# Kernel tuning notes

Hardware: AMD Instinct MI355X
Metric: run time of the kernel (lower is better)

## Reference

```python
import jax, jax.numpy as jnp
import numpy as np

B, T, D, H = 4, 4096, 2048, 16
HD = D // H
CAPACITY = 0.125
K = max(1, int(T * CAPACITY))  # 512
D_FF = int(D * 4 * 2 / 3)      # 5461
EPS = 1e-6


def setup_inputs() -> dict:
    key = jax.random.key(0)
    ks = jax.random.split(key, 9)
    s = 0.02
    return {
        "x": jax.random.normal(ks[0], (B, T, D), jnp.float32),
        "position_ids": jnp.tile(jnp.arange(T, dtype=jnp.int32)[None, :], (B, 1)),
        "router_w": jax.random.normal(ks[1], (D,), jnp.float32) * s,
        "norm1_w": jnp.ones((D,), jnp.float32),
        "qkv_w": jax.random.normal(ks[2], (D, 3 * D), jnp.float32) * s,
        "out_w": jax.random.normal(ks[3], (D, D), jnp.float32) * s,
        "norm2_w": jnp.ones((D,), jnp.float32),
        "w1": jax.random.normal(ks[4], (D, D_FF), jnp.float32) * s,
        "w2": jax.random.normal(ks[5], (D, D_FF), jnp.float32) * s,
        "w3": jax.random.normal(ks[6], (D_FF, D), jnp.float32) * s,
    }


def _rmsnorm(x, w):
    return x * jax.lax.rsqrt(jnp.mean(x * x, axis=-1, keepdims=True) + EPS) * w


def _block(x, pos, norm1_w, qkv_w, out_w, norm2_w, w1, w2, w3):
    # x: (B, k, D), pos: (B, k) original positions
    b, t, d = x.shape
    h = _rmsnorm(x, norm1_w)
    qkv = (h @ qkv_w).reshape(b, t, 3, H, HD)
    q = jnp.moveaxis(qkv[:, :, 0], 2, 1)  # (b, H, t, HD)
    k = jnp.moveaxis(qkv[:, :, 1], 2, 1)
    v = jnp.moveaxis(qkv[:, :, 2], 2, 1)
    attn = jnp.einsum("bhqd,bhkd->bhqk", q, k) / jnp.sqrt(jnp.float32(HD))
    # causal mask on ORIGINAL positions: query pos_i attends only to pos_j <= pos_i
    mask = (pos[:, :, None] < pos[:, None, :])[:, None]  # (b,1,t,t) True = masked
    attn = jnp.where(mask, -jnp.inf, attn)
    attn = jax.nn.softmax(attn, axis=-1)
    attn = jnp.nan_to_num(attn, nan=0.0)
    o = jnp.einsum("bhqk,bhkd->bhqd", attn, v)
    o = jnp.moveaxis(o, 1, 2).reshape(b, t, d) @ out_w
    x = x + o
    h = _rmsnorm(x, norm2_w)
    ff = (jax.nn.silu(h @ w1) * (h @ w2)) @ w3
    return x + ff


def reference(x, position_ids, router_w, norm1_w, qkv_w, out_w, norm2_w, w1, w2, w3):
    b, t, d = x.shape
    scores = x @ router_w  # (B, T)
    tie = jnp.arange(t, dtype=x.dtype) * 1e-6
    _, top_idx = jax.lax.top_k(scores + tie[None, :], K)
    sorted_idx = jnp.sort(top_idx, axis=-1)  # (B, K)
    x_sel = jnp.take_along_axis(x, sorted_idx[:, :, None], axis=1)  # (B, K, D)
    pos_sel = jnp.take_along_axis(position_ids, sorted_idx, axis=1)  # (B, K)
    x_proc = _block(x_sel, pos_sel, norm1_w, qkv_w, out_w, norm2_w, w1, w2, w3)
    b_idx = jnp.arange(b)[:, None]
    output = x.at[b_idx, sorted_idx].set(x_proc)
    return output
```

## Files before the change

kernel.cpp:

```cpp
#include <hip/hip_runtime.h>
#include <hip/hip_bf16.h>

#define BB 4
#define TT 4096
#define DD 2048
#define HH 16
#define HDD 128
#define KSEL 512
#define DFF 5461
#define DFFP 5504

typedef __attribute__((ext_vector_type(8))) short short8;
typedef __attribute__((ext_vector_type(4))) float floatx4;

__device__ __forceinline__ void g2l16(const void* g, void* l) {
  __builtin_amdgcn_global_load_lds((const __attribute__((address_space(1))) void*)g,
                                   (__attribute__((address_space(3))) void*)l,
                                   16, 0, 0);
}

__global__ __launch_bounds__(256) void router_copy(
    const float* __restrict__ x, const float* __restrict__ rw,
    float* __restrict__ out, float* __restrict__ scores) {
  const long row = blockIdx.x;
  const long base = row * DD;
  const int tid = threadIdx.x;
  float s = 0.f;
#pragma unroll
  for (int it = 0; it < 2; ++it) {
    const int c = (tid + it * 256) * 4;
    const float4 v = *(const float4*)(x + base + c);
    *(float4*)(out + base + c) = v;
    const float4 w = *(const float4*)(rw + c);
    s += v.x * w.x + v.y * w.y + v.z * w.z + v.w * w.w;
  }
  __shared__ float red[256];
  red[tid] = s; __syncthreads();
  for (int st = 128; st > 0; st >>= 1) { if (tid < st) red[tid] += red[tid + st]; __syncthreads(); }
  if (tid == 0) scores[row] = red[0];
}

__global__ __launch_bounds__(256) void topk_select(
    const float* __restrict__ scores, int* __restrict__ idx_sel) {
  const int b = blockIdx.x;
  const int tid = threadIdx.x;
  __shared__ float key[TT];
  __shared__ float fred[256];
  __shared__ int ired[256];
  __shared__ int ia[256], ib[256];
  __shared__ float s_lo, s_hi;
  __shared__ int s_strict;
  const float* sc = scores + (long)b * TT;
  for (int t = tid; t < TT; t += 256) key[t] = sc[t] + (float)t * 1e-6f;
  __syncthreads();
  float mn = 1e30f, mx = -1e30f;
  for (int t = tid; t < TT; t += 256) { const float v = key[t]; mn = fminf(mn, v); mx = fmaxf(mx, v); }
  fred[tid] = mn; __syncthreads();
  for (int s = 128; s > 0; s >>= 1) { if (tid < s) fred[tid] = fminf(fred[tid], fred[tid + s]); __syncthreads(); }
  if (tid == 0) s_lo = fred[0] - 1.f;
  __syncthreads();
  fred[tid] = mx; __syncthreads();
  for (int s = 128; s > 0; s >>= 1) { if (tid < s) fred[tid] = fmaxf(fred[tid], fred[tid + s]); __syncthreads(); }
  if (tid == 0) s_hi = fred[0];
  __syncthreads();
  for (int it = 0; it < 64; ++it) {
    const float lo = s_lo, hi = s_hi;
    const float mid = 0.5f * (lo + hi);
    if (!(mid > lo && mid < hi)) break;
    int c = 0;
    for (int t = tid; t < TT; t += 256) c += (key[t] > mid) ? 1 : 0;
    ired[tid] = c; __syncthreads();
    for (int s = 128; s > 0; s >>= 1) { if (tid < s) ired[tid] += ired[tid + s]; __syncthreads(); }
    if (tid == 0) { if (ired[0] >= KSEL) s_lo = mid; else s_hi = mid; }
    __syncthreads();
  }
  const float hi = s_hi;
  const int t0c = tid * 16;
  int cs = 0, ce = 0;
  for (int t = t0c; t < t0c + 16; ++t) { const float v = key[t]; cs += (v > hi); ce += (v == hi); }
  ia[tid] = cs; ib[tid] = ce; __syncthreads();
  if (tid == 0) {
    int st = 0, et = 0;
    for (int i2 = 0; i2 < 256; ++i2) { const int a = ia[i2], e2 = ib[i2]; ia[i2] = st; ib[i2] = et; st += a; et += e2; }
    s_strict = st;
  }
  __syncthreads();
  const int neq = KSEL - s_strict;
  {
    int eqr = ib[tid];
    int sel = 0;
    for (int t = t0c; t < t0c + 16; ++t) {
      const float v = key[t];
      if (v > hi) sel++;
      else if (v == hi) { if (eqr < neq) sel++; eqr++; }
    }
    ired[tid] = sel;
  }
  __syncthreads();
  if (tid == 0) { int st = 0; for (int i2 = 0; i2 < 256; ++i2) { const int a = ired[i2]; ired[i2] = st; st += a; } }
  __syncthreads();
  {
    int pos = ired[tid];
    int eqr = ib[tid];
    for (int t = t0c; t < t0c + 16; ++t) {
      const float v = key[t];
      bool s = false;
      if (v > hi) s = true;
      else if (v == hi) { s = (eqr < neq); eqr++; }
      if (s) idx_sel[(long)b * KSEL + (pos++)] = t;
    }
  }
}

__global__ __launch_bounds__(256) void rmsnorm_rows(
    const float* __restrict__ src, const int* __restrict__ idx,
    const float* __restrict__ w, __hip_bfloat16* __restrict__ dst, int gather) {
  const int m = blockIdx.x;
  const int tid = threadIdx.x;
  const float* row;
  if (gather) {
    const int b = m >> 9;
    const int t = idx[m];
    row = src + ((long)b * TT + t) * DD;
  } else {
    row = src + (long)m * DD;
  }
  const float4 v0 = *(const float4*)(row + tid * 4);
  const float4 v1 = *(const float4*)(row + 1024 + tid * 4);
  float ss = v0.x * v0.x + v0.y * v0.y + v0.z * v0.z + v0.w * v0.w
           + v1.x * v1.x + v1.y * v1.y + v1.z * v1.z + v1.w * v1.w;
  __shared__ float red[256];
  __shared__ float s_r;
  red[tid] = ss; __syncthreads();
  for (int s = 128; s > 0; s >>= 1) { if (tid < s) red[tid] += red[tid + s]; __syncthreads(); }
  if (tid == 0) s_r = rsqrtf(red[0] * (1.f / (float)DD) + 1e-6f);
  __syncthreads();
  const float r = s_r;
  const float4 w0 = *(const float4*)(w + tid * 4);
  const float4 w1v = *(const float4*)(w + 1024 + tid * 4);
  __hip_bfloat16* drow = dst + (long)m * DD;
  const int c = tid * 4;
  drow[c + 0] = __float2bfloat16(v0.x * r * w0.x);
  drow[c + 1] = __float2bfloat16(v0.y * r * w0.y);
  drow[c + 2] = __float2bfloat16(v0.z * r * w0.z);
  drow[c + 3] = __float2bfloat16(v0.w * r * w0.w);
  drow[1024 + c + 0] = __float2bfloat16(v1.x * r * w1v.x);
  drow[1024 + c + 1] = __float2bfloat16(v1.y * r * w1v.y);
  drow[1024 + c + 2] = __float2bfloat16(v1.z * r * w1v.z);
  drow[1024 + c + 3] = __float2bfloat16(v1.w * r * w1v.w);
}

__global__ __launch_bounds__(256) void transpose_cast(
    const float* __restrict__ in, __hip_bfloat16* __restrict__ out,
    int R, int C, int Rp, int Cp) {
  __shared__ float tile[32][33];
  const int r0 = blockIdx.x * 32, c0 = blockIdx.y * 32;
  const int tx = threadIdx.x & 31, ty = threadIdx.x >> 5;
  for (int yy = ty; yy < 32; yy += 8) {
    const int r = r0 + yy, c = c0 + tx;
    tile[yy][tx] = (r < R && c < C) ? in[(long)r * C + c] : 0.f;
  }
  __syncthreads();
  for (int yy = ty; yy < 32; yy += 8) {
    const int c = c0 + yy, r = r0 + tx;
    if (c < Cp && r < Rp) out[(long)c * Rp + r] = __float2bfloat16(tile[tx][yy]);
  }
}

__global__ __launch_bounds__(256) void softmax_rows(
    const __hip_bfloat16* __restrict__ S, __hip_bfloat16* __restrict__ P) {
  const int row = blockIdx.x * 4 + (threadIdx.x >> 6);
  const int lane = threadIdx.x & 63;
  const int i = row & (KSEL - 1);
  const long base = (long)row * KSEL;
  float v[8];
  float mx = -1e30f;
#pragma unroll
  for (int e = 0; e < 8; ++e) {
    const int j = e * 64 + lane;
    const float s = (j <= i) ? __bfloat162float(S[base + j]) : -1e30f;
    v[e] = s; mx = fmaxf(mx, s);
  }
#pragma unroll
  for (int d = 32; d > 0; d >>= 1) mx = fmaxf(mx, __shfl_xor(mx, d, 64));
  float sum = 0.f;
#pragma unroll
  for (int e = 0; e < 8; ++e) { const float p = __expf(v[e] - mx); v[e] = p; sum += p; }
#pragma unroll
  for (int d = 32; d > 0; d >>= 1) sum += __shfl_xor(sum, d, 64);
  const float inv = 1.f / sum;
#pragma unroll
  for (int e = 0; e < 8; ++e) P[base + e * 64 + lane] = __float2bfloat16(v[e] * inv);
}

template <int EPI>
__global__ __launch_bounds__(256) void gemm_bt(
    const __hip_bfloat16* __restrict__ A,
    const __hip_bfloat16* __restrict__ B,
    const __hip_bfloat16* __restrict__ B2,
    int ntm, int ntn, int gmx, int gnx,
    int K, long bsA, long bsB, float scale,
    void* __restrict__ out0,
    const int* __restrict__ idx,
    const float* __restrict__ xres,
    __hip_bfloat16* __restrict__ qb,
    __hip_bfloat16* __restrict__ kb,
    __hip_bfloat16* __restrict__ vtb) {
  constexpr bool DUAL = (EPI == 3);
  __shared__ unsigned short As[128 * 32];
  __shared__ unsigned short Bs[128 * 32];
  __shared__ unsigned short Bs2[DUAL ? 128 * 32 : 8];

  const int z = blockIdx.z;
  int bm, bn;
  if (gmx > 0) {
    const int xcd = blockIdx.x & 7;
    const int j = blockIdx.x >> 3;
    const int xm = xcd % gmx, xn = xcd / gmx;
    const int m_lo = (xm * ntm) / gmx;
    const int m_cnt = ((xm + 1) * ntm) / gmx - m_lo;
    const int n_lo = (xn * ntn) / gnx;
    const int n_cnt = ((xn + 1) * ntn) / gnx - n_lo;
    if (j >= m_cnt * n_cnt) return;
    bm = m_lo + j % m_cnt;
    bn = n_lo + j / m_cnt;
  } else {
    bm = blockIdx.x / ntn;
    bn = blockIdx.x % ntn;
  }
  const int tid = threadIdx.x;

  const __hip_bfloat16* Ab = A + (long)z * bsA + (long)bm * 128 * K;
  const __hip_bfloat16* Bb = B + (long)z * bsB + (long)bn * 128 * K;

  const int m1 = tid >> 2;
  const int p8 = (tid & 3) * 8;

  const floatx4 zero4 = {0.f, 0.f, 0.f, 0.f};
  floatx4 acc[4][4];
  floatx4 acc2[4][4];
#pragma unroll
  for (int i = 0; i < 4; ++i)
#pragma unroll
    for (int j = 0; j < 4; ++j) { acc[i][j] = zero4; if constexpr (DUAL) acc2[i][j] = zero4; }

  const int lane = tid & 63;
  const int wave = tid >> 6;
  const int wm = (wave & 1) << 6;
  const int wn = (wave >> 1) << 6;
  const int lrow = lane & 15;
  const int kq = (lane >> 4) << 3;

  for (int k0 = 0; k0 < K; k0 += 32) {
    const __hip_bfloat16* ag = Ab + (long)m1 * K + (k0 + p8);
    g2l16(ag, &As[tid * 8]);
    g2l16(ag + (long)64 * K, &As[(tid + 256) * 8]);
    const __hip_bfloat16* bg = Bb + (long)m1 * K + (k0 + p8);
    g2l16(bg, &Bs[tid * 8]);
    g2l16(bg + (long)64 * K, &Bs[(tid + 256) * 8]);
    if constexpr (DUAL) {
      const __hip_bfloat16* b2g = B2 + (long)bn * 128 * K + (long)m1 * K + (k0 + p8);
      g2l16(b2g, &Bs2[tid * 8]);
      g2l16(b2g + (long)64 * K, &Bs2[(tid + 256) * 8]);
    }
    __syncthreads();
    short8 af[4], bfr[4];
#pragma unroll
    for (int i = 0; i < 4; ++i) af[i] = *(const short8*)&As[(wm + i * 16 + lrow) * 32 + kq];
#pragma unroll
    for (int j = 0; j < 4; ++j) bfr[j] = *(const short8*)&Bs[(wn + j * 16 + lrow) * 32 + kq];
#pragma unroll
    for (int i = 0; i < 4; ++i)
#pragma unroll
      for (int j = 0; j < 4; ++j)
        acc[i][j] = __builtin_amdgcn_mfma_f32_16x16x32_bf16(af[i], bfr[j], acc[i][j], 0, 0, 0);
    if constexpr (DUAL) {
      short8 bf2[4];
#pragma unroll
      for (int j = 0; j < 4; ++j) bf2[j] = *(const short8*)&Bs2[(wn + j * 16 + lrow) * 32 + kq];
#pragma unroll
      for (int i = 0; i < 4; ++i)
#pragma unroll
        for (int j = 0; j < 4; ++j)
          acc2[i][j] = __builtin_amdgcn_mfma_f32_16x16x32_bf16(af[i], bf2[j], acc2[i][j], 0, 0, 0);
    }
    __syncthreads();
  }

  const int cn = lane & 15;
  const int rb = (lane >> 4) << 2;
#pragma unroll
  for (int i = 0; i < 4; ++i) {
#pragma unroll
    for (int j = 0; j < 4; ++j) {
#pragma unroll
      for (int r = 0; r < 4; ++r) {
        const int gm = bm * 128 + wm + i * 16 + rb + r;
        const int gn = bn * 128 + wn + j * 16 + cn;
        const float v = acc[i][j][r];
        if constexpr (EPI == 0) {
          ((__hip_bfloat16*)out0)[(long)z * KSEL * KSEL + (long)gm * KSEL + gn] =
              __float2bfloat16(v * scale);
        } else if constexpr (EPI == 5) {
          const int b = z >> 4, h = z & 15;
          ((__hip_bfloat16*)out0)[((long)(b * KSEL + gm)) * DD + h * HDD + gn] =
              __float2bfloat16(v);
        } else if constexpr (EPI == 1) {
          const int b = gm >> 9, t = gm & 511;
          const int sec = gn >> 11, rem = gn & 2047, h = rem >> 7, hd = rem & 127;
          const __hip_bfloat16 val = __float2bfloat16(v);
          const long bh = (long)b * HH + h;
          if (sec == 0)      qb[(bh * KSEL + t) * HDD + hd] = val;
          else if (sec == 1) kb[(bh * KSEL + t) * HDD + hd] = val;
          else               vtb[(bh * HDD + hd) * KSEL + t] = val;
        } else if constexpr (EPI == 2) {
          const int b = gm >> 9;
          const int t0 = idx[gm];
          ((float*)out0)[(long)gm * DD + gn] = xres[((long)b * TT + t0) * DD + gn] + v;
        } else if constexpr (EPI == 3) {
          const float a1 = v;
          const float a2 = acc2[i][j][r];
          const float sgl = a1 / (1.f + __expf(-a1));
          ((__hip_bfloat16*)out0)[(long)gm * DFFP + gn] = __float2bfloat16(sgl * a2);
        } else if constexpr (EPI == 4) {
          const int b = gm >> 9;
          const int t0 = idx[gm];
          ((float*)out0)[((long)b * TT + t0) * DD + gn] = xres[(long)gm * DD + gn] + v;
        }
      }
    }
  }
}

extern "C" void kernel_launch(void* const* d_in, const int* in_sizes, int n_in,
                              void* d_out, int out_size, void* d_ws, size_t ws_size,
                              hipStream_t stream) {
  const float* x        = (const float*)d_in[0];
  const float* router_w = (const float*)d_in[2];
  const float* norm1_w  = (const float*)d_in[3];
  const float* qkv_w    = (const float*)d_in[4];
  const float* out_w    = (const float*)d_in[5];
  const float* norm2_w  = (const float*)d_in[6];
  const float* w1       = (const float*)d_in[7];
  const float* w2       = (const float*)d_in[8];
  const float* w3       = (const float*)d_in[9];
  float* out = (float*)d_out;

  char* wsb = (char*)d_ws;
  size_t off = 0;
  auto alloc = [&](size_t bytes) -> void* {
    void* p = wsb + off;
    off += (bytes + 255) & ~(size_t)255;
    return p;
  };
  float* scores = (float*)alloc((size_t)BB * TT * 4);
  int* idxs     = (int*)alloc((size_t)BB * KSEL * 4);
  __hip_bfloat16* qkvt = (__hip_bfloat16*)alloc((size_t)3 * DD * DD * 2);
  __hip_bfloat16* outt = (__hip_bfloat16*)alloc((size_t)DD * DD * 2);
  __hip_bfloat16* w1t  = (__hip_bfloat16*)alloc((size_t)DFFP * DD * 2);
  __hip_bfloat16* w2t  = (__hip_bfloat16*)alloc((size_t)DFFP * DD * 2);
  __hip_bfloat16* w3t  = (__hip_bfloat16*)alloc((size_t)DD * DFFP * 2);
  __hip_bfloat16* h1   = (__hip_bfloat16*)alloc((size_t)BB * KSEL * DD * 2);
  __hip_bfloat16* qbuf = (__hip_bfloat16*)alloc((size_t)BB * HH * KSEL * HDD * 2);
  __hip_bfloat16* kbuf = (__hip_bfloat16*)alloc((size_t)BB * HH * KSEL * HDD * 2);
  __hip_bfloat16* vtb  = (__hip_bfloat16*)alloc((size_t)BB * HH * KSEL * HDD * 2);
  __hip_bfloat16* Sbuf = (__hip_bfloat16*)alloc((size_t)BB * HH * KSEL * KSEL * 2);
  __hip_bfloat16* Pbuf = (__hip_bfloat16*)alloc((size_t)BB * HH * KSEL * KSEL * 2);
  __hip_bfloat16* obuf = h1;
  __hip_bfloat16* h2   = qbuf;
  __hip_bfloat16* ubuf = Pbuf;
  float* x1f           = (float*)Sbuf;
  (void)ws_size; (void)in_sizes; (void)n_in; (void)out_size;

  const float inv_sqrt_hd = 0.08838834764831845f;

  router_copy<<<dim3(BB * TT), dim3(256), 0, stream>>>(x, router_w, out, scores);
  topk_select<<<dim3(BB), dim3(256), 0, stream>>>(scores, idxs);
  rmsnorm_rows<<<dim3(BB * KSEL), dim3(256), 0, stream>>>(x, idxs, norm1_w, h1, 1);
  transpose_cast<<<dim3(DD / 32, 3 * DD / 32), dim3(256), 0, stream>>>(qkv_w, qkvt, DD, 3 * DD, DD, 3 * DD);
  transpose_cast<<<dim3(DD / 32, DD / 32), dim3(256), 0, stream>>>(out_w, outt, DD, DD, DD, DD);
  transpose_cast<<<dim3(DD / 32, DFFP / 32), dim3(256), 0, stream>>>(w1, w1t, DD, DFF, DD, DFFP);
  transpose_cast<<<dim3(DD / 32, DFFP / 32), dim3(256), 0, stream>>>(w2, w2t, DD, DFF, DD, DFFP);
  transpose_cast<<<dim3(DFFP / 32, DD / 32), dim3(256), 0, stream>>>(w3, w3t, DFF, DD, DFFP, DD);
  gemm_bt<1><<<dim3(8 * 96, 1, 1), dim3(256), 0, stream>>>(
      h1, qkvt, nullptr, 16, 48, 2, 4, DD, 0, 0, 1.f, nullptr, nullptr, nullptr, qbuf, kbuf, vtb);
  gemm_bt<0><<<dim3(4 * 4, 1, BB * HH), dim3(256), 0, stream>>>(
      qbuf, kbuf, nullptr, 4, 4, 0, 0, HDD, (long)KSEL * HDD, (long)KSEL * HDD, inv_sqrt_hd,
      Sbuf, nullptr, nullptr, nullptr, nullptr, nullptr);
  softmax_rows<<<dim3(BB * HH * KSEL / 4), dim3(256), 0, stream>>>(Sbuf, Pbuf);
  gemm_bt<5><<<dim3(4, 1, BB * HH), dim3(256), 0, stream>>>(
      Pbuf, vtb, nullptr, 4, 1, 0, 0, KSEL, (long)KSEL * KSEL, (long)HDD * KSEL, 1.f,
      obuf, nullptr, nullptr, nullptr, nullptr, nullptr);
  gemm_bt<2><<<dim3(8 * 32, 1, 1), dim3(256), 0, stream>>>(
      obuf, outt, nullptr, 16, 16, 2, 4, DD, 0, 0, 1.f, x1f, idxs, x, nullptr, nullptr, nullptr);
  rmsnorm_rows<<<dim3(BB * KSEL), dim3(256), 0, stream>>>(x1f, nullptr, norm2_w, h2, 0);
  gemm_bt<3><<<dim3(8 * 88, 1, 1), dim3(256), 0, stream>>>(
      h2, w1t, w2t, 16, 43, 2, 4, DD, 0, 0, 1.f, ubuf, nullptr, nullptr, nullptr, nullptr, nullptr);
  gemm_bt<4><<<dim3(8 * 32, 1, 1), dim3(256), 0, stream>>>(
      ubuf, w3t, nullptr, 16, 16, 2, 4, DFFP, 0, 0, 1.f, out, idxs, x1f, nullptr, nullptr, nullptr);
}
```

Baseline: 1.060 ms.

## Add narrow-N GEMM tile variant and register-resident top-k selection

Templates the bf16 MFMA GEMM on its N tile width and switches the QKV, PV, out-proj, FFN up and FFN down GEMMs to 128x64 tiles, doubling the block count. Each wave then holds half the accumulators, which lowers register pressure and fills more CUs on the 512-row problems, at the cost of more A-tile reloads. The top-k kernel now keeps each thread's 16 scores in registers and uses wave shuffles instead of shared-memory tree reductions, cutting barriers in each bisection step.

```diff
diff --git a/kernel.cpp b/kernel.cpp
--- a/kernel.cpp
+++ b/kernel.cpp
@@ -44,40 +44,52 @@
     const float* __restrict__ scores, int* __restrict__ idx_sel) {
   const int b = blockIdx.x;
   const int tid = threadIdx.x;
-  __shared__ float key[TT];
-  __shared__ float fred[256];
-  __shared__ int ired[256];
-  __shared__ int ia[256], ib[256];
+  const int wave = tid >> 6, lane = tid & 63;
+  const float* sc = scores + (long)b * TT;
+  const int t0c = tid * 16;
+  float v[16];
+#pragma unroll
+  for (int e = 0; e < 16; ++e) v[e] = sc[t0c + e] + (float)(t0c + e) * 1e-6f;
+
+  __shared__ float smn[4], smx[4];
+  __shared__ int scnt[4];
   __shared__ float s_lo, s_hi;
   __shared__ int s_strict;
-  const float* sc = scores + (long)b * TT;
-  for (int t = tid; t < TT; t += 256) key[t] = sc[t] + (float)t * 1e-6f;
-  __syncthreads();
-  float mn = 1e30f, mx = -1e30f;
-  for (int t = tid; t < TT; t += 256) { const float v = key[t]; mn = fminf(mn, v); mx = fmaxf(mx, v); }
-  fred[tid] = mn; __syncthreads();
-  for (int s = 128; s > 0; s >>= 1) { if (tid < s) fred[tid] = fminf(fred[tid], fred[tid + s]); __syncthreads(); }
-  if (tid == 0) s_lo = fred[0] - 1.f;
-  __syncthreads();
-  fred[tid] = mx; __syncthreads();
-  for (int s = 128; s > 0; s >>= 1) { if (tid < s) fred[tid] = fmaxf(fred[tid], fred[tid + s]); __syncthreads(); }
-  if (tid == 0) s_hi = fred[0];
+  __shared__ int ia[256], ib[256], ired[256];
+
+  float mn = v[0], mx = v[0];
+#pragma unroll
+  for (int e = 1; e < 16; ++e) { mn = fminf(mn, v[e]); mx = fmaxf(mx, v[e]); }
+#pragma unroll
+  for (int d = 32; d > 0; d >>= 1) { mn = fminf(mn, __shfl_xor(mn, d, 64)); mx = fmaxf(mx, __shfl_xor(mx, d, 64)); }
+  if (lane == 0) { smn[wave] = mn; smx[wave] = mx; }
+  __syncthreads();
+  if (tid == 0) {
+    s_lo = fminf(fminf(smn[0], smn[1]), fminf(smn[2], smn[3])) - 1.f;
+    s_hi = fmaxf(fmaxf(smx[0], smx[1]), fmaxf(smx[2], smx[3]));
+  }
   __syncthreads();
   for (int it = 0; it < 64; ++it) {
     const float lo = s_lo, hi = s_hi;
     const float mid = 0.5f * (lo + hi);
     if (!(mid > lo && mid < hi)) break;
     int c = 0;
-    for (int t = tid; t < TT; t += 256) c += (key[t] > mid) ? 1 : 0;
-    ired[tid] = c; __syncthreads();
-    for (int s = 128; s > 0; s >>= 1) { if (tid < s) ired[tid] += ired[tid + s]; __syncthreads(); }
-    if (tid == 0) { if (ired[0] >= KSEL) s_lo = mid; else s_hi = mid; }
+#pragma unroll
+    for (int e = 0; e < 16; ++e) c += (v[e] > mid) ? 1 : 0;
+#pragma unroll
+    for (int d = 32; d > 0; d >>= 1) c += __shfl_xor(c, d, 64);
+    if (lane == 0) scnt[wave] = c;
     __syncthreads();
+    if (tid == 0) {
+      const int tot = scnt[0] + scnt[1] + scnt[2] + scnt[3];
+      if (tot >= KSEL) s_lo = mid; else s_hi = mid;
+    }
+    __syncthreads();
   }
   const float hi = s_hi;
-  const int t0c = tid * 16;
   int cs = 0, ce = 0;
-  for (int t = t0c; t < t0c + 16; ++t) { const float v = key[t]; cs += (v > hi); ce += (v == hi); }
+#pragma unroll
+  for (int e = 0; e < 16; ++e) { cs += (v[e] > hi); ce += (v[e] == hi); }
   ia[tid] = cs; ib[tid] = ce; __syncthreads();
   if (tid == 0) {
     int st = 0, et = 0;
@@ -89,10 +101,10 @@
   {
     int eqr = ib[tid];
     int sel = 0;
-    for (int t = t0c; t < t0c + 16; ++t) {
-      const float v = key[t];
-      if (v > hi) sel++;
-      else if (v == hi) { if (eqr < neq) sel++; eqr++; }
+#pragma unroll
+    for (int e = 0; e < 16; ++e) {
+      if (v[e] > hi) sel++;
+      else if (v[e] == hi) { if (eqr < neq) sel++; eqr++; }
     }
     ired[tid] = sel;
   }
@@ -102,12 +114,12 @@
   {
     int pos = ired[tid];
     int eqr = ib[tid];
-    for (int t = t0c; t < t0c + 16; ++t) {
-      const float v = key[t];
+#pragma unroll
+    for (int e = 0; e < 16; ++e) {
       bool s = false;
-      if (v > hi) s = true;
-      else if (v == hi) { s = (eqr < neq); eqr++; }
-      if (s) idx_sel[(long)b * KSEL + (pos++)] = t;
+      if (v[e] > hi) s = true;
+      else if (v[e] == hi) { s = (eqr < neq); eqr++; }
+      if (s) idx_sel[(long)b * KSEL + (pos++)] = t0c + e;
     }
   }
 }
@@ -193,7 +205,7 @@
   for (int e = 0; e < 8; ++e) P[base + e * 64 + lane] = __float2bfloat16(v[e] * inv);
 }
 
-template <int EPI>
+template <int EPI, int BN>
 __global__ __launch_bounds__(256) void gemm_bt(
     const __hip_bfloat16* __restrict__ A,
     const __hip_bfloat16* __restrict__ B,
@@ -207,9 +219,11 @@
     __hip_bfloat16* __restrict__ kb,
     __hip_bfloat16* __restrict__ vtb) {
   constexpr bool DUAL = (EPI == 3);
+  constexpr int WN = (BN == 128) ? 64 : 32;
+  constexpr int NJ = WN / 16;
   __shared__ unsigned short As[128 * 32];
-  __shared__ unsigned short Bs[128 * 32];
-  __shared__ unsigned short Bs2[DUAL ? 128 * 32 : 8];
+  __shared__ unsigned short Bs[BN * 32];
+  __shared__ unsigned short Bs2[DUAL ? BN * 32 : 8];
 
   const int z = blockIdx.z;
   int bm, bn;
@@ -231,23 +245,23 @@
   const int tid = threadIdx.x;
 
   const __hip_bfloat16* Ab = A + (long)z * bsA + (long)bm * 128 * K;
-  const __hip_bfloat16* Bb = B + (long)z * bsB + (long)bn * 128 * K;
+  const __hip_bfloat16* Bb = B + (long)z * bsB + (long)bn * BN * K;
 
   const int m1 = tid >> 2;
   const int p8 = (tid & 3) * 8;
 
   const floatx4 zero4 = {0.f, 0.f, 0.f, 0.f};
-  floatx4 acc[4][4];
-  floatx4 acc2[4][4];
+  floatx4 acc[4][NJ];
+  floatx4 acc2[DUAL ? 4 : 1][DUAL ? NJ : 1];
 #pragma unroll
   for (int i = 0; i < 4; ++i)
 #pragma unroll
-    for (int j = 0; j < 4; ++j) { acc[i][j] = zero4; if constexpr (DUAL) acc2[i][j] = zero4; }
+    for (int j = 0; j < NJ; ++j) { acc[i][j] = zero4; if constexpr (DUAL) acc2[i][j] = zero4; }
 
   const int lane = tid & 63;
   const int wave = tid >> 6;
   const int wm = (wave & 1) << 6;
-  const int wn = (wave >> 1) << 6;
+  const int wn = (wave >> 1) * WN;
   const int lrow = lane & 15;
   const int kq = (lane >> 4) << 3;
 
@@ -257,31 +271,31 @@
     g2l16(ag + (long)64 * K, &As[(tid + 256) * 8]);
     const __hip_bfloat16* bg = Bb + (long)m1 * K + (k0 + p8);
     g2l16(bg, &Bs[tid * 8]);
-    g2l16(bg + (long)64 * K, &Bs[(tid + 256) * 8]);
+    if constexpr (BN == 128) g2l16(bg + (long)64 * K, &Bs[(tid + 256) * 8]);
     if constexpr (DUAL) {
-      const __hip_bfloat16* b2g = B2 + (long)bn * 128 * K + (long)m1 * K + (k0 + p8);
+      const __hip_bfloat16* b2g = B2 + (long)bn * BN * K + (long)m1 * K + (k0 + p8);
       g2l16(b2g, &Bs2[tid * 8]);
-      g2l16(b2g + (long)64 * K, &Bs2[(tid + 256) * 8]);
+      if constexpr (BN == 128) g2l16(b2g + (long)64 * K, &Bs2[(tid + 256) * 8]);
     }
     __syncthreads();
-    short8 af[4], bfr[4];
+    short8 af[4], bfr[NJ];
 #pragma unroll
     for (int i = 0; i < 4; ++i) af[i] = *(const short8*)&As[(wm + i * 16 + lrow) * 32 + kq];
 #pragma unroll
-    for (int j = 0; j < 4; ++j) bfr[j] = *(const short8*)&Bs[(wn + j * 16 + lrow) * 32 + kq];
+    for (int j = 0; j < NJ; ++j) bfr[j] = *(const short8*)&Bs[(wn + j * 16 + lrow) * 32 + kq];
 #pragma unroll
     for (int i = 0; i < 4; ++i)
 #pragma unroll
-      for (int j = 0; j < 4; ++j)
+      for (int j = 0; j < NJ; ++j)
         acc[i][j] = __builtin_amdgcn_mfma_f32_16x16x32_bf16(af[i], bfr[j], acc[i][j], 0, 0, 0);
     if constexpr (DUAL) {
-      short8 bf2[4];
-#pragma unroll
-      for (int j = 0; j < 4; ++j) bf2[j] = *(const short8*)&Bs2[(wn + j * 16 + lrow) * 32 + kq];
+      short8 bf2[NJ];
+#pragma unroll
+      for (int j = 0; j < NJ; ++j) bf2[j] = *(const short8*)&Bs2[(wn + j * 16 + lrow) * 32 + kq];
 #pragma unroll
       for (int i = 0; i < 4; ++i)
 #pragma unroll
-        for (int j = 0; j < 4; ++j)
+        for (int j = 0; j < NJ; ++j)
           acc2[i][j] = __builtin_amdgcn_mfma_f32_16x16x32_bf16(af[i], bf2[j], acc2[i][j], 0, 0, 0);
     }
     __syncthreads();
@@ -292,11 +306,11 @@
 #pragma unroll
   for (int i = 0; i < 4; ++i) {
 #pragma unroll
-    for (int j = 0; j < 4; ++j) {
+    for (int j = 0; j < NJ; ++j) {
 #pragma unroll
       for (int r = 0; r < 4; ++r) {
         const int gm = bm * 128 + wm + i * 16 + rb + r;
-        const int gn = bn * 128 + wn + j * 16 + cn;
+        const int gn = bn * BN + wn + j * 16 + cn;
         const float v = acc[i][j][r];
         if constexpr (EPI == 0) {
           ((__hip_bfloat16*)out0)[(long)z * KSEL * KSEL + (long)gm * KSEL + gn] =
@@ -382,20 +396,20 @@
   transpose_cast<<<dim3(DD / 32, DFFP / 32), dim3(256), 0, stream>>>(w1, w1t, DD, DFF, DD, DFFP);
   transpose_cast<<<dim3(DD / 32, DFFP / 32), dim3(256), 0, stream>>>(w2, w2t, DD, DFF, DD, DFFP);
   transpose_cast<<<dim3(DFFP / 32, DD / 32), dim3(256), 0, stream>>>(w3, w3t, DFF, DD, DFFP, DD);
-  gemm_bt<1><<<dim3(8 * 96, 1, 1), dim3(256), 0, stream>>>(
-      h1, qkvt, nullptr, 16, 48, 2, 4, DD, 0, 0, 1.f, nullptr, nullptr, nullptr, qbuf, kbuf, vtb);
-  gemm_bt<0><<<dim3(4 * 4, 1, BB * HH), dim3(256), 0, stream>>>(
+  gemm_bt<1, 64><<<dim3(8 * 192, 1, 1), dim3(256), 0, stream>>>(
+      h1, qkvt, nullptr, 16, 96, 2, 4, DD, 0, 0, 1.f, nullptr, nullptr, nullptr, qbuf, kbuf, vtb);
+  gemm_bt<0, 128><<<dim3(4 * 4, 1, BB * HH), dim3(256), 0, stream>>>(
       qbuf, kbuf, nullptr, 4, 4, 0, 0, HDD, (long)KSEL * HDD, (long)KSEL * HDD, inv_sqrt_hd,
       Sbuf, nullptr, nullptr, nullptr, nullptr, nullptr);
   softmax_rows<<<dim3(BB * HH * KSEL / 4), dim3(256), 0, stream>>>(Sbuf, Pbuf);
-  gemm_bt<5><<<dim3(4, 1, BB * HH), dim3(256), 0, stream>>>(
-      Pbuf, vtb, nullptr, 4, 1, 0, 0, KSEL, (long)KSEL * KSEL, (long)HDD * KSEL, 1.f,
+  gemm_bt<5, 64><<<dim3(8, 1, BB * HH), dim3(256), 0, stream>>>(
+      Pbuf, vtb, nullptr, 4, 2, 0, 0, KSEL, (long)KSEL * KSEL, (long)HDD * KSEL, 1.f,
       obuf, nullptr, nullptr, nullptr, nullptr, nullptr);
-  gemm_bt<2><<<dim3(8 * 32, 1, 1), dim3(256), 0, stream>>>(
-      obuf, outt, nullptr, 16, 16, 2, 4, DD, 0, 0, 1.f, x1f, idxs, x, nullptr, nullptr, nullptr);
+  gemm_bt<2, 64><<<dim3(8 * 64, 1, 1), dim3(256), 0, stream>>>(
+      obuf, outt, nullptr, 16, 32, 2, 4, DD, 0, 0, 1.f, x1f, idxs, x, nullptr, nullptr, nullptr);
   rmsnorm_rows<<<dim3(BB * KSEL), dim3(256), 0, stream>>>(x1f, nullptr, norm2_w, h2, 0);
-  gemm_bt<3><<<dim3(8 * 88, 1, 1), dim3(256), 0, stream>>>(
-      h2, w1t, w2t, 16, 43, 2, 4, DD, 0, 0, 1.f, ubuf, nullptr, nullptr, nullptr, nullptr, nullptr);
-  gemm_bt<4><<<dim3(8 * 32, 1, 1), dim3(256), 0, stream>>>(
-      ubuf, w3t, nullptr, 16, 16, 2, 4, DFFP, 0, 0, 1.f, out, idxs, x1f, nullptr, nullptr, nullptr);
-}
+  gemm_bt<3, 64><<<dim3(8 * 176, 1, 1), dim3(256), 0, stream>>>(
+      h2, w1t, w2t, 16, 86, 2, 4, DD, 0, 0, 1.f, ubuf, nullptr, nullptr, nullptr, nullptr, nullptr);
+  gemm_bt<4, 64><<<dim3(8 * 64, 1, 1), dim3(256), 0, stream>>>(
+      ubuf, w3t, nullptr, 16, 32, 2, 4, DFFP, 0, 0, 1.f, out, idxs, x1f, nullptr, nullptr, nullptr);
+}
```

After: 920.0 us. 13.2% less time.
